# Performance work log

Hardware: AMD Instinct MI355X
Metric: run time of the kernel (lower is better)

The kernel has to match this reference:

```python
import jax, jax.numpy as jnp
import numpy as np

N_NODES = 50000
HEADS = 4
CH = 128
NEG_SLOPE = 0.2


def _gatv2_layer(x, src, dst, Wl, Wr, att, bias):
    # x: [N, Fin]; src/dst: [E'] (self-loops already appended)
    N = x.shape[0]
    xl = (x @ Wl).reshape(N, HEADS, CH)   # source-side transform
    xr = (x @ Wr).reshape(N, HEADS, CH)   # target-side transform
    e = jax.nn.leaky_relu(xl[src] + xr[dst], NEG_SLOPE)   # [E', H, C]
    logits = jnp.einsum('ehc,hc->eh', e, att)             # [E', H]
    # segment softmax over incoming edges of each destination node
    m = jax.ops.segment_max(logits, dst, num_segments=N)
    m = jnp.where(jnp.isfinite(m), m, 0.0)
    p = jnp.exp(logits - m[dst])
    denom = jax.ops.segment_sum(p, dst, num_segments=N)
    alpha = p / denom[dst]                                # [E', H]
    out = jax.ops.segment_sum(alpha[:, :, None] * xl[src], dst, num_segments=N)
    return out.reshape(N, HEADS * CH) + bias


def setup_inputs() -> dict:
    key = jax.random.key(0)
    ks = jax.random.split(key, 12)
    E = 400000
    x = jax.random.normal(ks[0], (N_NODES, 55), dtype=jnp.float32)
    edge_index = jax.random.randint(ks[1], (2, E), 0, N_NODES, dtype=jnp.int64)
    s = 0.1
    d1, d2 = 55, HEADS * CH
    return {
        'x': x,
        'edge_index': edge_index,
        'W1l': jax.random.normal(ks[2], (d1, d2), dtype=jnp.float32) * s,
        'W1r': jax.random.normal(ks[3], (d1, d2), dtype=jnp.float32) * s,
        'att1': jax.random.normal(ks[4], (HEADS, CH), dtype=jnp.float32) * s,
        'b1': jnp.zeros((d2,), dtype=jnp.float32),
        'W2l': jax.random.normal(ks[5], (d2, d2), dtype=jnp.float32) * s,
        'W2r': jax.random.normal(ks[6], (d2, d2), dtype=jnp.float32) * s,
        'att2': jax.random.normal(ks[7], (HEADS, CH), dtype=jnp.float32) * s,
        'b2': jnp.zeros((d2,), dtype=jnp.float32),
        'Wc': jax.random.normal(ks[8], (d2, 49), dtype=jnp.float32) * s,
        'bc': jnp.zeros((49,), dtype=jnp.float32),
    }


def reference(x, edge_index, W1l, W1r, att1, b1, W2l, W2r, att2, b2, Wc, bc):
    # add self loops once (PyG GATv2Conv default add_self_loops=True)
    loops = jnp.arange(N_NODES, dtype=edge_index.dtype)
    src = jnp.concatenate([edge_index[0], loops])
    dst = jnp.concatenate([edge_index[1], loops])
    h = _gatv2_layer(x, src, dst, W1l, W1r, att1, b1)
    h = jax.nn.elu(h)  # dropout is identity in eval mode
    h = _gatv2_layer(h, src, dst, W2l, W2r, att2, b2)
    h = jax.nn.elu(h)
    # forward applies conv2 a second time (conv3 unused in source)
    h = _gatv2_layer(h, src, dst, W2l, W2r, att2, b2)
    h = jax.nn.elu(h)
    return h @ Wc + bc
```

## Files before the change

kernel.cpp:

```cpp
#include <hip/hip_runtime.h>
#include <hip/hip_bf16.h>

constexpr int NN   = 50000;
constexpr int EE   = 400000;
constexpr int EP   = 450000;
constexpr int D    = 512;
constexpr int D2   = 1024;
constexpr int F0   = 55;
constexpr int F0P  = 64;
constexpr int OUTC = 49;

typedef __hip_bfloat16 bf16;

using frag_ab = __attribute__((ext_vector_type(8))) short;
using frag_cd = __attribute__((ext_vector_type(4))) float;

__device__ inline void stf(float* p, float v) { *p = v; }
__device__ inline void stf(bf16* p, float v)  { *p = __float2bfloat16(v); }

union BV { uint4 u; __hip_bfloat162 h[4]; };
__device__ inline void unpack8(const BV& b, float* f) {
    #pragma unroll
    for (int j = 0; j < 4; ++j) {
        float2 t = __bfloat1622float2(b.h[j]);
        f[2 * j] = t.x; f[2 * j + 1] = t.y;
    }
}

template <typename TC>
__global__ __launch_bounds__(256) void gemm_mfma_bt(
    const bf16* __restrict__ A,
    const bf16* __restrict__ Bt,
    TC* __restrict__ C,
    const float* __restrict__ bias,
    int M, int Ncs, int K)
{
    constexpr int BM = 128, BN = 128, BK = 32;
    __shared__ bf16 As[BM * BK];
    __shared__ bf16 Bs[BN * BK];

    const int tid  = threadIdx.x;
    const int wave = tid >> 6;
    const int lane = tid & 63;
    const int rowBase = blockIdx.y * BM;
    const int colBase = blockIdx.x * BN;

    frag_cd acc[4][4] = {};

    int arow0 = rowBase + wave * 32 + (lane >> 2);
    int arow1 = arow0 + 16;
    if (arow0 >= M) arow0 = M - 1;
    if (arow1 >= M) arow1 = M - 1;
    const bf16* gA0 = A + (size_t)arow0 * K + (lane & 3) * 8;
    const bf16* gA1 = A + (size_t)arow1 * K + (lane & 3) * 8;
    const int brow0 = colBase + wave * 32 + (lane >> 2);
    const bf16* gB0 = Bt + (size_t)brow0 * K + (lane & 3) * 8;
    const bf16* gB1 = gB0 + (size_t)16 * K;

    bf16* lA0 = &As[(wave * 32)      * BK];
    bf16* lA1 = &As[(wave * 32 + 16) * BK];
    bf16* lB0 = &Bs[(wave * 32)      * BK];
    bf16* lB1 = &Bs[(wave * 32 + 16) * BK];

    const int m  = lane & 15;
    const int kq = lane >> 4;
    const int wm = (wave >> 1) * 64;
    const int wn = (wave & 1) * 64;

    for (int k0 = 0; k0 < K; k0 += BK) {
        __builtin_amdgcn_global_load_lds(
            (const __attribute__((address_space(1))) void*)(gA0 + k0),
            (__attribute__((address_space(3))) void*)lA0, 16, 0, 0);
        __builtin_amdgcn_global_load_lds(
            (const __attribute__((address_space(1))) void*)(gA1 + k0),
            (__attribute__((address_space(3))) void*)lA1, 16, 0, 0);
        __builtin_amdgcn_global_load_lds(
            (const __attribute__((address_space(1))) void*)(gB0 + k0),
            (__attribute__((address_space(3))) void*)lB0, 16, 0, 0);
        __builtin_amdgcn_global_load_lds(
            (const __attribute__((address_space(1))) void*)(gB1 + k0),
            (__attribute__((address_space(3))) void*)lB1, 16, 0, 0);
        __syncthreads();

        frag_ab a[4], b[4];
        #pragma unroll
        for (int i = 0; i < 4; ++i)
            a[i] = *(const frag_ab*)&As[(wm + i * 16 + m) * BK + kq * 8];
        #pragma unroll
        for (int j = 0; j < 4; ++j)
            b[j] = *(const frag_ab*)&Bs[(wn + j * 16 + m) * BK + kq * 8];
        #pragma unroll
        for (int i = 0; i < 4; ++i)
            #pragma unroll
            for (int j = 0; j < 4; ++j)
                acc[i][j] = __builtin_amdgcn_mfma_f32_16x16x32_bf16(
                    a[i], b[j], acc[i][j], 0, 0, 0);
        __syncthreads();
    }

    #pragma unroll
    for (int i = 0; i < 4; ++i) {
        #pragma unroll
        for (int r = 0; r < 4; ++r) {
            int row = rowBase + wm + i * 16 + kq * 4 + r;
            if (row >= M) continue;
            #pragma unroll
            for (int j = 0; j < 4; ++j) {
                int col = colBase + wn + j * 16 + m;
                if (col >= Ncs) continue;
                float v = acc[i][j][r];
                if (bias) v += bias[col];
                stf(&C[(size_t)row * Ncs + col], v);
            }
        }
    }
}

__global__ void convert_transpose(const float* __restrict__ W, bf16* __restrict__ Wt,
                                  int K, int N) {
    __shared__ float tile[32][33];
    int bn = blockIdx.x * 32, bk = blockIdx.y * 32;
    int tx = threadIdx.x & 31, ty = threadIdx.x >> 5;
    #pragma unroll
    for (int i = 0; i < 32; i += 8)
        tile[ty + i][tx] = W[(size_t)(bk + ty + i) * N + bn + tx];
    __syncthreads();
    #pragma unroll
    for (int i = 0; i < 32; i += 8)
        Wt[(size_t)(bn + ty + i) * K + bk + tx] = __float2bfloat16(tile[tx][ty + i]);
}

__global__ void pad_convert_x(const float* __restrict__ x, bf16* __restrict__ Xp) {
    int idx = blockIdx.x * blockDim.x + threadIdx.x;
    if (idx >= NN * F0P) return;
    int n = idx >> 6, t = idx & 63;
    float v = (t < F0) ? x[n * F0 + t] : 0.f;
    Xp[idx] = __float2bfloat16(v);
}

__global__ void conv_transpose_w1(const float* __restrict__ W, bf16* __restrict__ Wt) {
    int n = blockIdx.x;
    int k = threadIdx.x;
    float v = (k < F0) ? W[(size_t)k * D + n] : 0.f;
    Wt[n * F0P + k] = __float2bfloat16(v);
}

__global__ void conv_transpose_wc(const float* __restrict__ W, bf16* __restrict__ Wt) {
    int n = blockIdx.x;
    for (int k = threadIdx.x; k < D; k += blockDim.x) {
        float v = (n < OUTC) ? W[(size_t)k * OUTC + n] : 0.f;
        Wt[(size_t)n * D + k] = __float2bfloat16(v);
    }
}

__global__ void zero_ints(int* __restrict__ p, int n) {
    int i = blockIdx.x * blockDim.x + threadIdx.x;
    if (i < n) p[i] = 0;
}

__global__ void count_dst(const int* __restrict__ dstIdx, int* __restrict__ cnt) {
    int e = blockIdx.x * blockDim.x + threadIdx.x;
    if (e >= EP) return;
    int dst = (e < EE) ? dstIdx[e] : (e - EE);
    atomicAdd(&cnt[dst], 1);
}

__global__ void scan_blocks(const int* __restrict__ cnt, int* __restrict__ off,
                            int* __restrict__ bsum) {
    __shared__ int sh[1024];
    int i = blockIdx.x * 1024 + threadIdx.x;
    int v = (i < NN) ? cnt[i] : 0;
    sh[threadIdx.x] = v;
    __syncthreads();
    #pragma unroll
    for (int d = 1; d < 1024; d <<= 1) {
        int t = (threadIdx.x >= d) ? sh[threadIdx.x - d] : 0;
        __syncthreads();
        sh[threadIdx.x] += t;
        __syncthreads();
    }
    if (i < NN) off[i] = sh[threadIdx.x] - v;
    if (threadIdx.x == 1023) bsum[blockIdx.x] = sh[1023];
}

__global__ void scan_bsums(int* __restrict__ bsum, int* __restrict__ bbase,
                           int* __restrict__ off, int nb) {
    int lane = threadIdx.x;
    int orig = (lane < nb) ? bsum[lane] : 0;
    int v = orig;
    #pragma unroll
    for (int d = 1; d < 64; d <<= 1) {
        int t = __shfl_up(v, d);
        if (lane >= d) v += t;
    }
    if (lane < nb) bbase[lane] = v - orig;
    if (lane == 63) off[NN] = v;
}

__global__ void add_base(int* __restrict__ off, const int* __restrict__ bbase) {
    int i = blockIdx.x * 1024 + threadIdx.x;
    if (blockIdx.x == 0 || i >= NN) return;
    off[i] += bbase[blockIdx.x];
}

__global__ void fill_srcpos(const int* __restrict__ srcIdx, const int* __restrict__ dstIdx,
                            const int* __restrict__ off, int* __restrict__ cnt,
                            int* __restrict__ srcPos) {
    int e = blockIdx.x * blockDim.x + threadIdx.x;
    if (e >= EP) return;
    int dst = (e < EE) ? dstIdx[e] : (e - EE);
    int src = (e < EE) ? srcIdx[e] : (e - EE);
    int pos = off[dst] + atomicAdd(&cnt[dst], 1);
    srcPos[pos] = src;
}

__global__ __launch_bounds__(256) void gat_edge_fused(
    const bf16* __restrict__ XLR, const float* __restrict__ att,
    const int* __restrict__ off, const int* __restrict__ srcPos,
    const float* __restrict__ bias, bf16* __restrict__ Hout)
{
    int v = blockIdx.x * 4 + (threadIdx.x >> 6);
    if (v >= NN) return;
    int lane = threadIdx.x & 63;

    BV rb; rb.u = *(const uint4*)(XLR + (size_t)v * D2 + D + lane * 8);
    float xr[8]; unpack8(rb, xr);
    const float4* a4 = (const float4*)(att + lane * 8);
    float4 aa = a4[0], ab = a4[1];
    float at[8] = {aa.x, aa.y, aa.z, aa.w, ab.x, ab.y, ab.z, ab.w};

    int s0 = off[v], s1 = off[v + 1];
    float m = -1e30f, den = 0.f;
    float acc[8] = {};
    for (int i = s0; i < s1; ++i) {
        int src = srcPos[i];
        BV lb; lb.u = *(const uint4*)(XLR + (size_t)src * D2 + lane * 8);
        float xl[8]; unpack8(lb, xl);
        float s = 0.f;
        #pragma unroll
        for (int j = 0; j < 8; ++j) {
            float t = xl[j] + xr[j];
            t = t > 0.f ? t : 0.2f * t;
            s += t * at[j];
        }
        s += __shfl_xor(s, 1);
        s += __shfl_xor(s, 2);
        s += __shfl_xor(s, 4);
        s += __shfl_xor(s, 8);
        float mn = fmaxf(m, s);
        float scale = __expf(m - mn);
        float p = __expf(s - mn);
        den = den * scale + p;
        #pragma unroll
        for (int j = 0; j < 8; ++j) acc[j] = acc[j] * scale + p * xl[j];
        m = mn;
    }
    float r = 1.f / den;

    const float4* b4 = (const float4*)(bias + lane * 8);
    float4 ba = b4[0], bb = b4[1];
    float bi[8] = {ba.x, ba.y, ba.z, ba.w, bb.x, bb.y, bb.z, bb.w};
    BV ob;
    #pragma unroll
    for (int j = 0; j < 4; ++j) {
        float o0 = acc[2 * j] * r + bi[2 * j];
        float o1 = acc[2 * j + 1] * r + bi[2 * j + 1];
        o0 = o0 > 0.f ? o0 : (__expf(o0) - 1.f);
        o1 = o1 > 0.f ? o1 : (__expf(o1) - 1.f);
        ob.h[j] = __hip_bfloat162{__float2bfloat16(o0), __float2bfloat16(o1)};
    }
    *(uint4*)(Hout + (size_t)v * D + lane * 8) = ob.u;
}

extern "C" void kernel_launch(void* const* d_in, const int* in_sizes, int n_in,
                              void* d_out, int out_size, void* d_ws, size_t ws_size,
                              hipStream_t stream) {
    const float* x    = (const float*)d_in[0];
    const int*   ei   = (const int*)d_in[1];
    const float* W1l  = (const float*)d_in[2];
    const float* W1r  = (const float*)d_in[3];
    const float* att1 = (const float*)d_in[4];
    const float* b1   = (const float*)d_in[5];
    const float* W2l  = (const float*)d_in[6];
    const float* W2r  = (const float*)d_in[7];
    const float* att2 = (const float*)d_in[8];
    const float* b2   = (const float*)d_in[9];
    const float* Wc   = (const float*)d_in[10];
    const float* bc   = (const float*)d_in[11];
    float* out = (float*)d_out;

    const int* srcIdx = ei;
    const int* dstIdx = ei + EE;

    constexpr int NB = (NN + 1023) / 1024;

    bf16* XLR  = (bf16*)d_ws;
    bf16* Hb   = XLR + (size_t)NN * D2;
    bf16* Xpad = Hb + (size_t)NN * D;
    bf16* W2T  = Xpad + (size_t)NN * F0P;
    bf16* W1T  = W2T + (size_t)D2 * D;
    bf16* WcT  = W1T + (size_t)D2 * F0P;
    int* cnt   = (int*)(WcT + (size_t)128 * D);
    int* cnt2  = cnt + NN;
    int* off   = cnt2 + NN;
    int* srcPos= off + (NN + 1);
    int* bsum  = srcPos + EP;
    int* bbase = bsum + NB;

    zero_ints<<<(2 * NN + 255) / 256, 256, 0, stream>>>(cnt, 2 * NN);
    count_dst<<<(EP + 255) / 256, 256, 0, stream>>>(dstIdx, cnt);
    scan_blocks<<<NB, 1024, 0, stream>>>(cnt, off, bsum);
    scan_bsums<<<1, 64, 0, stream>>>(bsum, bbase, off, NB);
    add_base<<<NB, 1024, 0, stream>>>(off, bbase);
    fill_srcpos<<<(EP + 255) / 256, 256, 0, stream>>>(srcIdx, dstIdx, off, cnt2, srcPos);

    dim3 ctGrid(D / 32, D / 32);
    convert_transpose<<<ctGrid, 256, 0, stream>>>(W2l, W2T, D, D);
    convert_transpose<<<ctGrid, 256, 0, stream>>>(W2r, W2T + (size_t)D * D, D, D);
    conv_transpose_w1<<<D, F0P, 0, stream>>>(W1l, W1T);
    conv_transpose_w1<<<D, F0P, 0, stream>>>(W1r, W1T + (size_t)D * F0P);
    conv_transpose_wc<<<128, 256, 0, stream>>>(Wc, WcT);
    pad_convert_x<<<(NN * F0P + 255) / 256, 256, 0, stream>>>(x, Xpad);

    dim3 gemmGrid(D2 / 128, (NN + 127) / 128);
    int nodeBlocks = (NN + 3) / 4;

    gemm_mfma_bt<bf16><<<gemmGrid, 256, 0, stream>>>(Xpad, W1T, XLR, nullptr, NN, D2, F0P);
    gat_edge_fused<<<nodeBlocks, 256, 0, stream>>>(XLR, att1, off, srcPos, b1, Hb);

    for (int rep = 0; rep < 2; ++rep) {
        gemm_mfma_bt<bf16><<<gemmGrid, 256, 0, stream>>>(Hb, W2T, XLR, nullptr, NN, D2, D);
        gat_edge_fused<<<nodeBlocks, 256, 0, stream>>>(XLR, att2, off, srcPos, b2, Hb);
    }

    dim3 gridc(1, (NN + 127) / 128);
    gemm_mfma_bt<float><<<gridc, 256, 0, stream>>>(Hb, WcT, out, bc, NN, OUTC, D);
}
```

Before: 659.4 us.

## Prefetch gathered source rows in edge kernel and swizzle GEMM block order

The per-node edge loop now software-pipelines the gathers of source-row features, keeping the next two neighbour rows in flight while the current one is processed. This is meant to hide the latency of the dependent srcPos-then-XLR loads. Separately, the 8-column GEMM remaps its block IDs so each run of 64 consecutive blocks covers 8 row tiles by all 8 column tiles, aiming for better cache reuse of A and B tiles. The GEMM grid is padded with extra blocks that exit early. The bf16 pack and unpack helpers are rewritten without a union, with no intended behaviour change.

```diff
diff --git a/kernel.cpp b/kernel.cpp
--- a/kernel.cpp
+++ b/kernel.cpp
@@ -18,11 +18,12 @@
 __device__ inline void stf(float* p, float v) { *p = v; }
 __device__ inline void stf(bf16* p, float v)  { *p = __float2bfloat16(v); }
 
-union BV { uint4 u; __hip_bfloat162 h[4]; };
-__device__ inline void unpack8(const BV& b, float* f) {
+__device__ inline void unpack8(uint4 u, float* f) {
+    unsigned w[4] = {u.x, u.y, u.z, u.w};
     #pragma unroll
     for (int j = 0; j < 4; ++j) {
-        float2 t = __bfloat1622float2(b.h[j]);
+        __hip_bfloat162 h = *(__hip_bfloat162*)&w[j];
+        float2 t = __bfloat1622float2(h);
         f[2 * j] = t.x; f[2 * j + 1] = t.y;
     }
 }
@@ -39,11 +40,19 @@
     __shared__ bf16 As[BM * BK];
     __shared__ bf16 Bs[BN * BK];
 
+    int bx = blockIdx.x, by = blockIdx.y;
+    if (gridDim.x == 8) {
+        int bid = by * 8 + bx;
+        bx = (bid >> 3) & 7;
+        by = (bid & 7) + ((bid >> 6) << 3);
+        if (by * BM >= M) return;
+    }
+
     const int tid  = threadIdx.x;
     const int wave = tid >> 6;
     const int lane = tid & 63;
-    const int rowBase = blockIdx.y * BM;
-    const int colBase = blockIdx.x * BN;
+    const int rowBase = by * BM;
+    const int colBase = bx * BN;
 
     frag_cd acc[4][4] = {};
 
@@ -223,8 +232,8 @@
     if (v >= NN) return;
     int lane = threadIdx.x & 63;
 
-    BV rb; rb.u = *(const uint4*)(XLR + (size_t)v * D2 + D + lane * 8);
-    float xr[8]; unpack8(rb, xr);
+    uint4 ru = *(const uint4*)(XLR + (size_t)v * D2 + D + lane * 8);
+    float xr[8]; unpack8(ru, xr);
     const float4* a4 = (const float4*)(att + lane * 8);
     float4 aa = a4[0], ab = a4[1];
     float at[8] = {aa.x, aa.y, aa.z, aa.w, ab.x, ab.y, ab.z, ab.w};
@@ -232,10 +241,18 @@
     int s0 = off[v], s1 = off[v + 1];
     float m = -1e30f, den = 0.f;
     float acc[8] = {};
+
+    uint4 lb0 = {0, 0, 0, 0}, lb1 = {0, 0, 0, 0};
+    if (s0 < s1)     lb0 = *(const uint4*)(XLR + (size_t)srcPos[s0] * D2 + lane * 8);
+    if (s0 + 1 < s1) lb1 = *(const uint4*)(XLR + (size_t)srcPos[s0 + 1] * D2 + lane * 8);
+
     for (int i = s0; i < s1; ++i) {
-        int src = srcPos[i];
-        BV lb; lb.u = *(const uint4*)(XLR + (size_t)src * D2 + lane * 8);
-        float xl[8]; unpack8(lb, xl);
+        uint4 cur = lb0;
+        lb0 = lb1;
+        if (i + 2 < s1)
+            lb1 = *(const uint4*)(XLR + (size_t)srcPos[i + 2] * D2 + lane * 8);
+
+        float xl[8]; unpack8(cur, xl);
         float s = 0.f;
         #pragma unroll
         for (int j = 0; j < 8; ++j) {
@@ -260,16 +277,18 @@
     const float4* b4 = (const float4*)(bias + lane * 8);
     float4 ba = b4[0], bb = b4[1];
     float bi[8] = {ba.x, ba.y, ba.z, ba.w, bb.x, bb.y, bb.z, bb.w};
-    BV ob;
+    uint4 ou;
+    unsigned* ow = (unsigned*)&ou;
     #pragma unroll
     for (int j = 0; j < 4; ++j) {
         float o0 = acc[2 * j] * r + bi[2 * j];
         float o1 = acc[2 * j + 1] * r + bi[2 * j + 1];
         o0 = o0 > 0.f ? o0 : (__expf(o0) - 1.f);
         o1 = o1 > 0.f ? o1 : (__expf(o1) - 1.f);
-        ob.h[j] = __hip_bfloat162{__float2bfloat16(o0), __float2bfloat16(o1)};
-    }
-    *(uint4*)(Hout + (size_t)v * D + lane * 8) = ob.u;
+        __hip_bfloat162 h{__float2bfloat16(o0), __float2bfloat16(o1)};
+        ow[j] = *(unsigned*)&h;
+    }
+    *(uint4*)(Hout + (size_t)v * D + lane * 8) = ou;
 }
 
 extern "C" void kernel_launch(void* const* d_in, const int* in_sizes, int n_in,
@@ -322,7 +341,7 @@
     conv_transpose_wc<<<128, 256, 0, stream>>>(Wc, WcT);
     pad_convert_x<<<(NN * F0P + 255) / 256, 256, 0, stream>>>(x, Xpad);
 
-    dim3 gemmGrid(D2 / 128, (NN + 127) / 128);
+    dim3 gemmGrid(D2 / 128, ((NN + 127) / 128 + 7) / 8 * 8 + 8);
     int nodeBlocks = (NN + 3) / 4;
 
     gemm_mfma_bt<bf16><<<gemmGrid, 256, 0, stream>>>(Xpad, W1T, XLR, nullptr, NN, D2, F0P);
```

New measurement: 640.8 us. -2.8%, faster.
